# Performance work log

Measured on AMD Instinct MI355X. Metric: run time of the kernel, lower is better.

## Reference

```python
import jax, jax.numpy as jnp
import numpy as np
from jax import lax

DN = ('NCHW', 'OIHW', 'NCHW')

def _conv(x, w, b):
    # Conv2d(k=4, stride=2, padding=1): H -> H/2
    y = lax.conv_general_dilated(x, w, (2, 2), ((1, 1), (1, 1)), dimension_numbers=DN)
    return y + b[None, :, None, None]

def _deconv(x, w, b):
    # ConvTranspose2d(k=4, stride=2, padding=1): H -> 2H.
    # Equivalent dense conv: flip kernel spatially, swap in/out channels,
    # lhs_dilation = stride, padding = k-1-p = 2.
    wf = jnp.flip(w, (2, 3)).transpose(1, 0, 2, 3)  # (out, in, 4, 4)
    y = lax.conv_general_dilated(x, wf, (1, 1), ((2, 2), (2, 2)), lhs_dilation=(2, 2), dimension_numbers=DN)
    return y + b[None, :, None, None]

def setup_inputs() -> dict:
    key = jax.random.key(0)
    ks = jax.random.split(key, 20)
    f = jnp.float32
    s = 0.05  # small init scale for stability
    inp = {
        'x':   jax.random.uniform(ks[0], (64, 3, 224, 224), dtype=f),
        # encoder conv weights (OIHW) + biases
        'ew1': jax.random.normal(ks[1], (32, 3, 4, 4), f) * s,   'eb1': jnp.zeros((32,), f),
        'ew2': jax.random.normal(ks[2], (64, 32, 4, 4), f) * s,  'eb2': jnp.zeros((64,), f),
        'ew3': jax.random.normal(ks[3], (128, 64, 4, 4), f) * s, 'eb3': jnp.zeros((128,), f),
        'ew4': jax.random.normal(ks[4], (64, 128, 4, 4), f) * s, 'eb4': jnp.zeros((64,), f),
        # codebook: uniform(-1/K, 1/K) like torch init, K=4000, D=12544
        'emb': jax.random.uniform(ks[5], (4000, 12544), f, -1.0 / 4000, 1.0 / 4000),
        # decoder conv-transpose weights in torch layout (in, out, kh, kw) + biases
        'dw1': jax.random.normal(ks[6], (64, 128, 4, 4), f) * s, 'db1': jnp.zeros((128,), f),
        'dw2': jax.random.normal(ks[7], (128, 64, 4, 4), f) * s, 'db2': jnp.zeros((64,), f),
        'dw3': jax.random.normal(ks[8], (64, 32, 4, 4), f) * s,  'db3': jnp.zeros((32,), f),
        'dw4': jax.random.normal(ks[9], (32, 3, 4, 4), f) * s,   'db4': jnp.zeros((3,), f),
    }
    return inp

def reference(x, ew1, eb1, ew2, eb2, ew3, eb3, ew4, eb4, emb,
              dw1, db1, dw2, db2, dw3, db3, dw4, db4):
    sg = lax.stop_gradient
    B = x.shape[0]
    # ---- Encoder ----
    h = jax.nn.relu(_conv(x, ew1, eb1))
    h = jax.nn.relu(_conv(h, ew2, eb2))
    h = jax.nn.relu(_conv(h, ew3, eb3))
    h = _conv(h, ew4, eb4)                 # (B, 64, 14, 14)
    z = h.reshape(B, -1)                   # (B, 12544)
    # ---- Vector quantization ----
    # ||z||^2 - 2 z E^T + ||e||^2, argmin over codebook
    dist = (jnp.sum(z * z, axis=1, keepdims=True)
            - 2.0 * (z @ emb.T)
            + jnp.sum(emb * emb, axis=1))  # (B, 4000)
    idx = jnp.argmin(dist, axis=1)         # (B,)
    quantized = emb[idx]                   # (B, 12544) -- direct gather (== onehot @ emb)
    e_latent = jnp.mean((sg(quantized) - z) ** 2)
    q_latent = jnp.mean((quantized - sg(z)) ** 2)
    vq_loss = q_latent + 0.25 * e_latent
    zq = z + sg(quantized - z)             # straight-through
    # ---- Decoder ----
    d = zq.reshape(B, 64, 14, 14)
    d = jax.nn.relu(_deconv(d, dw1, db1))
    d = jax.nn.relu(_deconv(d, dw2, db2))
    d = jax.nn.relu(_deconv(d, dw3, db3))
    x_recon = jax.nn.sigmoid(_deconv(d, dw4, db4))  # (B, 3, 224, 224)
    recon_loss = jnp.mean((x_recon - x) ** 2)
    loss = recon_loss + vq_loss
    return (x_recon, loss, recon_loss, vq_loss)
```

## Files before the change

### kernel.cpp

```cpp
#include <hip/hip_runtime.h>
#include <math.h>

typedef unsigned short u16;
typedef unsigned int u32;
typedef __attribute__((ext_vector_type(8))) short short8;
typedef __attribute__((ext_vector_type(4))) float f32x4;

__device__ __forceinline__ u16 f2bf(float f) {
    u32 u = __float_as_uint(f);
    u = u + 0x7fffu + ((u >> 16) & 1u);
    return (u16)(u >> 16);
}
__device__ __forceinline__ float bf2f(u16 h) { return __uint_as_float(((u32)h) << 16); }

__device__ __forceinline__ f32x4 mfma16(short8 a, short8 b, f32x4 c) {
    return __builtin_amdgcn_mfma_f32_16x16x32_bf16(a, b, c, 0, 0, 0);
}

__device__ __forceinline__ uint4 pack8(float4 a, float4 b) {
    uint4 r;
    r.x = (u32)f2bf(a.x) | ((u32)f2bf(a.y) << 16);
    r.y = (u32)f2bf(a.z) | ((u32)f2bf(a.w) << 16);
    r.z = (u32)f2bf(b.x) | ((u32)f2bf(b.y) << 16);
    r.w = (u32)f2bf(b.z) | ((u32)f2bf(b.w) << 16);
    return r;
}

__global__ __launch_bounds__(256) void prep_conv_w(
    const float* __restrict__ w, u16* __restrict__ o, int CIN, int COUT)
{
    int i = blockIdx.x * 256 + threadIdx.x;
    int tot = CIN * 16 * COUT;
    if (i >= tot) return;
    int j = i & 7; int r = i >> 3;
    int co = r % COUT; int r2 = r / COUT;
    int tap = r2 & 15; int ch = r2 >> 4;
    int ci = ch * 8 + j;
    o[i] = f2bf(w[((size_t)co * CIN + ci) * 16 + tap]);
}
__global__ __launch_bounds__(256) void prep_deconv_w(
    const float* __restrict__ w, u16* __restrict__ o, int CIN, int COUT, int COPAD)
{
    int i = blockIdx.x * 256 + threadIdx.x;
    int tot = CIN * 16 * COPAD;
    if (i >= tot) return;
    int j = i & 7; int r = i >> 3;
    int co = r % COPAD; int r2 = r / COPAD;
    int t16 = r2 & 15; int ch = r2 >> 4;
    int py = t16 >> 3, px = (t16 >> 2) & 1, qq = t16 & 3;
    int ta = qq >> 1, tb = qq & 1;
    int ky = py + 2 * ta, kx = px + 2 * tb;
    int ci = ch * 8 + j;
    o[i] = (co < COUT) ? f2bf(w[(((size_t)ci * COUT + co) * 16) + ky * 4 + kx]) : (u16)0;
}
__global__ __launch_bounds__(256) void prep_conv1_w(
    const float* __restrict__ w, u16* __restrict__ o)
{
    int i = blockIdx.x * 256 + threadIdx.x;
    if (i >= 2048) return;
    int j = i & 7; int kx = j >> 1, cp = j & 1;
    int r = i >> 3;
    int co = r & 31; int r2 = r >> 5;
    int ky = r2 & 3; int h = r2 >> 2;
    int ci = 2 * h + cp;
    o[i] = (ci < 3) ? f2bf(w[((co * 3 + ci) * 16) + ky * 4 + kx]) : (u16)0;
}

template<int CIN, int COUT, int COTILE, int H2, int W2, int NSEG, int MB,
         int MBW, int NWF, int RELU, int STOREZ>
__global__ __launch_bounds__(256) void conv_mfma(
    const u16* __restrict__ in, const u16* __restrict__ wcvt,
    const float* __restrict__ bias, u16* __restrict__ outp,
    float* __restrict__ z32)
{
    constexpr int CHUNKS = CIN / 8, CGI = CIN / 8, CGO = COUT / 8;
    constexpr int HIN = H2 * 2, WIN = W2 * 2, SLOTW = 35;
    constexpr int NF = COTILE / 16, WM = MB / MBW, WN = NF / NWF;
    static_assert(WM * WN == 4, "wave layout");
    constexpr int TBu = MB * 4 * SLOTW, WBu = 16 * COTILE;
    constexpr int EBu = (MB * 16 * COTILE * 2 + 15) / 16;
    constexpr int SM = (TBu + WBu) > EBu ? (TBu + WBu) : EBu;
    __shared__ uint4 smem[SM];
    uint4* T = smem; uint4* wS = smem + TBu;
    u16* E = (u16*)smem;

    const int tid = threadIdx.x, wid = tid >> 6, lane = tid & 63;
    const int q = lane >> 4, lm = lane & 15;
    const int wm = wid / WN, wn = wid % WN;
    const int cobase = blockIdx.y * COTILE;
    const int mbase = blockIdx.x * MB;

    f32x4 acc[MBW][NWF];
    #pragma unroll
    for (int a = 0; a < MBW; ++a)
        #pragma unroll
        for (int b = 0; b < NWF; ++b) {
            acc[a][b][0] = 0.f; acc[a][b][1] = 0.f;
            acc[a][b][2] = 0.f; acc[a][b][3] = 0.f;
        }

    for (int ch = 0; ch < CHUNKS; ++ch) {
        __syncthreads();
        for (int i = tid; i < TBu; i += 256) {
            int mb = i / (4 * SLOTW), r2 = i % (4 * SLOTW);
            int r = r2 / SLOTW, s = r2 % SLOTW;
            int mbg = mbase + mb;
            int n = mbg / (H2 * NSEG), rr = mbg % (H2 * NSEG);
            int oy = rr / NSEG, ox0 = (rr % NSEG) << 4;
            int iy = 2 * oy - 1 + r, ix = 2 * ox0 - 1 + s;
            uint4 v = {0u, 0u, 0u, 0u};
            if ((unsigned)iy < (unsigned)HIN && (unsigned)ix < (unsigned)WIN)
                v = *(const uint4*)(in + (size_t)(((n * CGI + ch) * HIN + iy) * WIN + ix) * 8);
            T[i] = v;
        }
        for (int i = tid; i < WBu; i += 256) {
            int tap = i / COTILE, co = i % COTILE;
            wS[i] = *(const uint4*)(wcvt + (size_t)((ch * 16 + tap) * COUT + cobase + co) * 8);
        }
        __syncthreads();
        #pragma unroll
        for (int ky = 0; ky < 4; ++ky) {
            short8 Af[MBW]; short8 Bf[NWF];
            #pragma unroll
            for (int im = 0; im < MBW; ++im) {
                int mb = wm * MBW + im;
                Af[im] = *(const short8*)(T + (mb * 4 + ky) * SLOTW + 2 * lm + q);
            }
            #pragma unroll
            for (int inf = 0; inf < NWF; ++inf)
                Bf[inf] = *(const short8*)(wS + (ky * 4 + q) * COTILE + wn * NWF * 16 + inf * 16 + lm);
            #pragma unroll
            for (int im = 0; im < MBW; ++im)
                #pragma unroll
                for (int inf = 0; inf < NWF; ++inf)
                    acc[im][inf] = mfma16(Af[im], Bf[inf], acc[im][inf]);
        }
    }
    __syncthreads();
    #pragma unroll
    for (int inf = 0; inf < NWF; ++inf) {
        int col = wn * NWF * 16 + inf * 16 + lm;
        float bv = bias[cobase + col];
        #pragma unroll
        for (int im = 0; im < MBW; ++im) {
            int pixb = (wm * MBW + im) * 16 + q * 4;
            #pragma unroll
            for (int r = 0; r < 4; ++r) {
                float v = acc[im][inf][r] + bv;
                if (RELU) v = fmaxf(v, 0.f);
                E[(pixb + r) * COTILE + col] = f2bf(v);
            }
        }
    }
    __syncthreads();
    for (int i = tid; i < MB * 16 * (COTILE / 8); i += 256) {
        int pix = i / (COTILE / 8), cg = i % (COTILE / 8);
        int mb = pix >> 4, m = pix & 15;
        int mbg = mbase + mb;
        int n = mbg / (H2 * NSEG), rr = mbg % (H2 * NSEG);
        int oy = rr / NSEG, ox0 = (rr % NSEG) << 4;
        int ox = ox0 + m;
        if (ox < W2)
            *(uint4*)(outp + (size_t)(((n * CGO + cobase / 8 + cg) * H2 + oy) * W2 + ox) * 8) =
                *(uint4*)(E + pix * COTILE + cg * 8);
    }
    if (STOREZ) {
        for (int i = tid; i < MB * 16 * COTILE; i += 256) {
            int pix = i / COTILE, co = i % COTILE;
            int mb = pix >> 4, m = pix & 15;
            int mbg = mbase + mb;
            int n = mbg / (H2 * NSEG), rr = mbg % (H2 * NSEG);
            int oy = rr / NSEG, ox0 = (rr % NSEG) << 4;
            int ox = ox0 + m;
            if (ox < W2)
                z32[(size_t)((n * COUT + cobase + co) * H2 + oy) * W2 + ox] =
                    bf2f(E[pix * COTILE + co]);
        }
    }
}

__global__ __launch_bounds__(256) void conv1_mfma(
    const float* __restrict__ x, const u16* __restrict__ w1c,
    const float* __restrict__ bias, u16* __restrict__ outp)
{
    constexpr int MB = 16, MBW = 4, NWF = 2, COTILE = 32, W2 = 112, H2 = 112, NSEG = 7;
    constexpr int TBu = MB * 2 * 64, WBu = 256;
    __shared__ uint4 smem[TBu + WBu];
    uint4* T1 = smem; uint4* w1S = smem + TBu;
    u16* E = (u16*)smem;

    const int tid = threadIdx.x, wid = tid >> 6, lane = tid & 63;
    const int q = lane >> 4, lm = lane & 15;
    const int wm = wid;
    const int mbase = blockIdx.x * MB;

    f32x4 acc[MBW][NWF];
    #pragma unroll
    for (int a = 0; a < MBW; ++a)
        #pragma unroll
        for (int b = 0; b < NWF; ++b) {
            acc[a][b][0] = 0.f; acc[a][b][1] = 0.f;
            acc[a][b][2] = 0.f; acc[a][b][3] = 0.f;
        }

    for (int i = tid; i < TBu; i += 256) {
        int mb = i >> 7; int r = i & 127;
        int h = r >> 6; int r2 = r & 63;
        int ky = r2 >> 4; int m = r2 & 15;
        int mbg = mbase + mb;
        int n = mbg / (H2 * NSEG), rr = mbg % (H2 * NSEG);
        int oy = rr / NSEG, ox0 = (rr % NSEG) << 4;
        int iy = 2 * oy - 1 + ky;
        int ixb = 2 * (ox0 + m) - 1;
        u32 u[4];
        #pragma unroll
        for (int kx = 0; kx < 4; ++kx) {
            float v0 = 0.f, v1 = 0.f;
            int ix = ixb + kx;
            if ((unsigned)iy < 224u && (unsigned)ix < 224u) {
                int ci0 = 2 * h;
                v0 = x[((size_t)(n * 3 + ci0) * 224 + iy) * 224 + ix];
                if (ci0 + 1 < 3) v1 = x[((size_t)(n * 3 + ci0 + 1) * 224 + iy) * 224 + ix];
            }
            u[kx] = (u32)f2bf(v0) | ((u32)f2bf(v1) << 16);
        }
        uint4 vv; vv.x = u[0]; vv.y = u[1]; vv.z = u[2]; vv.w = u[3];
        T1[i] = vv;
    }
    if (tid < 256) {
        w1S[tid] = *(const uint4*)(w1c + (size_t)tid * 8);
    }
    __syncthreads();
    #pragma unroll
    for (int h = 0; h < 2; ++h) {
        short8 Af[MBW]; short8 Bf[NWF];
        #pragma unroll
        for (int im = 0; im < MBW; ++im) {
            int mb = wm * MBW + im;
            Af[im] = *(const short8*)(T1 + (mb * 2 + h) * 64 + lane);
        }
        #pragma unroll
        for (int inf = 0; inf < NWF; ++inf)
            Bf[inf] = *(const short8*)(w1S + (h * 4 + q) * 32 + inf * 16 + lm);
        #pragma unroll
        for (int im = 0; im < MBW; ++im)
            #pragma unroll
            for (int inf = 0; inf < NWF; ++inf)
                acc[im][inf] = mfma16(Af[im], Bf[inf], acc[im][inf]);
    }
    __syncthreads();
    #pragma unroll
    for (int inf = 0; inf < NWF; ++inf) {
        int col = inf * 16 + lm;
        float bv = bias[col];
        #pragma unroll
        for (int im = 0; im < MBW; ++im) {
            int pixb = (wm * MBW + im) * 16 + q * 4;
            #pragma unroll
            for (int r = 0; r < 4; ++r) {
                float v = fmaxf(acc[im][inf][r] + bv, 0.f);
                E[(pixb + r) * COTILE + col] = f2bf(v);
            }
        }
    }
    __syncthreads();
    for (int i = tid; i < MB * 16 * (COTILE / 8); i += 256) {
        int pix = i / (COTILE / 8), cg = i % (COTILE / 8);
        int mb = pix >> 4, m = pix & 15;
        int mbg = mbase + mb;
        int n = mbg / (H2 * NSEG), rr = mbg % (H2 * NSEG);
        int oy = rr / NSEG, ox0 = (rr % NSEG) << 4;
        int ox = ox0 + m;
        *(uint4*)(outp + (size_t)(((n * 4 + cg) * H2 + oy) * W2 + ox) * 8) =
            *(uint4*)(E + pix * COTILE + cg * 8);
    }
}

template<int CIN, int COUT, int COPAD, int COTILE, int Hp, int Wp, int NSEG,
         int MB, int MBW, int NWF, int RELU>
__global__ __launch_bounds__(256) void deconv_mfma(
    const u16* __restrict__ in, const u16* __restrict__ dcvt,
    const float* __restrict__ bias, u16* __restrict__ outp)
{
    constexpr int CHUNKS = CIN / 8, CGI = CIN / 8, CGO = COUT / 8;
    constexpr int SLOTW = 17;
    constexpr int NF = COTILE / 16, WM = MB / MBW, WN = NF / NWF;
    static_assert(WM * WN == 4, "wave layout");
    constexpr int BPP = 64 * Hp * NSEG / MB;
    constexpr int TBu = MB * 2 * SLOTW, WBu = 4 * COTILE;
    constexpr int EBu = (MB * 16 * COTILE * 2 + 15) / 16;
    constexpr int SM = (TBu + WBu) > EBu ? (TBu + WBu) : EBu;
    __shared__ uint4 smem[SM];
    uint4* T = smem; uint4* wS = smem + TBu;
    u16* E = (u16*)smem;

    const int tid = threadIdx.x, wid = tid >> 6, lane = tid & 63;
    const int q = lane >> 4, lm = lane & 15;
    const int wm = wid / WN, wn = wid % WN;
    const int par = blockIdx.x / BPP;
    const int py = par >> 1, px = par & 1;
    const int mbase = (blockIdx.x % BPP) * MB;
    const int cobase = blockIdx.y * COTILE;

    f32x4 acc[MBW][NWF];
    #pragma unroll
    for (int a = 0; a < MBW; ++a)
        #pragma unroll
        for (int b = 0; b < NWF; ++b) {
            acc[a][b][0] = 0.f; acc[a][b][1] = 0.f;
            acc[a][b][2] = 0.f; acc[a][b][3] = 0.f;
        }

    for (int ch = 0; ch < CHUNKS; ++ch) {
        __syncthreads();
        for (int i = tid; i < TBu; i += 256) {
            int mb = i / (2 * SLOTW), r2 = i % (2 * SLOTW);
            int rr_ = r2 / SLOTW, s = r2 % SLOTW;
            int mbg = mbase + mb;
            int n = mbg / (Hp * NSEG), rm = mbg % (Hp * NSEG);
            int oyp = rm / NSEG, u0 = (rm % NSEG) << 4;
            int iy = oyp + (1 - py) - 1 + rr_;
            int ix = u0 + (1 - px) - 1 + s;
            uint4 v = {0u, 0u, 0u, 0u};
            if ((unsigned)iy < (unsigned)Hp && (unsigned)ix < (unsigned)Wp)
                v = *(const uint4*)(in + (size_t)(((n * CGI + ch) * Hp + iy) * Wp + ix) * 8);
            T[i] = v;
        }
        for (int i = tid; i < WBu; i += 256) {
            int qq = i / COTILE, co = i % COTILE;
            wS[i] = *(const uint4*)(dcvt + (size_t)((ch * 16 + par * 4 + qq) * COPAD + cobase + co) * 8);
        }
        __syncthreads();
        {
            short8 Af[MBW]; short8 Bf[NWF];
            #pragma unroll
            for (int im = 0; im < MBW; ++im) {
                int mb = wm * MBW + im;
                Af[im] = *(const short8*)(T + (mb * 2 + (1 - (q >> 1))) * SLOTW + lm + 1 - (q & 1));
            }
            #pragma unroll
            for (int inf = 0; inf < NWF; ++inf)
                Bf[inf] = *(const short8*)(wS + q * COTILE + wn * NWF * 16 + inf * 16 + lm);
            #pragma unroll
            for (int im = 0; im < MBW; ++im)
                #pragma unroll
                for (int inf = 0; inf < NWF; ++inf)
                    acc[im][inf] = mfma16(Af[im], Bf[inf], acc[im][inf]);
        }
    }
    __syncthreads();
    #pragma unroll
    for (int inf = 0; inf < NWF; ++inf) {
        int col = wn * NWF * 16 + inf * 16 + lm;
        float bv = bias[cobase + col];
        #pragma unroll
        for (int im = 0; im < MBW; ++im) {
            int pixb = (wm * MBW + im) * 16 + q * 4;
            #pragma unroll
            for (int r = 0; r < 4; ++r) {
                float v = acc[im][inf][r] + bv;
                if (RELU) v = fmaxf(v, 0.f);
                E[(pixb + r) * COTILE + col] = f2bf(v);
            }
        }
    }
    __syncthreads();
    for (int i = tid; i < MB * 16 * (COTILE / 8); i += 256) {
        int pix = i / (COTILE / 8), cg = i % (COTILE / 8);
        int mb = pix >> 4, m = pix & 15;
        int mbg = mbase + mb;
        int n = mbg / (Hp * NSEG), rm = mbg % (Hp * NSEG);
        int oyp = rm / NSEG, u0 = (rm % NSEG) << 4;
        int u = u0 + m;
        if (u < Wp) {
            int ox = 2 * u + (px ? 0 : 1);
            int oy = 2 * oyp + (py ? 0 : 1);
            *(uint4*)(outp + (size_t)(((n * CGO + cobase / 8 + cg) * (2 * Hp) + oy) * (2 * Wp) + ox) * 8) =
                *(uint4*)(E + pix * COTILE + cg * 8);
        }
    }
}

__global__ __launch_bounds__(256) void deconv4_mfma(
    const u16* __restrict__ in, const u16* __restrict__ dcvt,
    const float* __restrict__ bias, float* __restrict__ outp,
    const float* __restrict__ xref, float* __restrict__ bpart)
{
    constexpr int Hp = 112, Wp = 112, NSEG = 7, MB = 16, MBW = 4;
    constexpr int CGI = 4, CHUNKS = 4, COPAD = 16;
    constexpr int TROW = 3, TCOL = 18;
    constexpr int TBu = MB * TROW * TCOL;
    constexpr int WBu = CHUNKS * 16 * COPAD / 16 * 16;
    __shared__ uint4 smem[TBu + 1024];
    __shared__ float red[4];
    uint4* T = smem; uint4* wS = smem + TBu;

    const int tid = threadIdx.x, wid = tid >> 6, lane = tid & 63;
    const int q = lane >> 4, lm = lane & 15;
    const int wm = wid;
    const int mbase = blockIdx.x * MB;

    f32x4 acc[4][MBW];
    #pragma unroll
    for (int p = 0; p < 4; ++p)
        #pragma unroll
        for (int a = 0; a < MBW; ++a) {
            acc[p][a][0] = 0.f; acc[p][a][1] = 0.f; acc[p][a][2] = 0.f; acc[p][a][3] = 0.f;
        }

    for (int i = tid; i < 1024; i += 256)
        wS[i] = *(const uint4*)(dcvt + (size_t)i * 8);

    for (int ch = 0; ch < CHUNKS; ++ch) {
        __syncthreads();
        for (int i = tid; i < TBu; i += 256) {
            int mb = i / (TROW * TCOL), r2 = i % (TROW * TCOL);
            int r = r2 / TCOL, s = r2 % TCOL;
            int mbg = mbase + mb;
            int n = mbg / (Hp * NSEG), rm = mbg % (Hp * NSEG);
            int oyp = rm / NSEG, u0 = (rm % NSEG) << 4;
            int iy = oyp - 1 + r;
            int ix = u0 - 1 + s;
            uint4 v = {0u, 0u, 0u, 0u};
            if ((unsigned)iy < (unsigned)Hp && (unsigned)ix < (unsigned)Wp)
                v = *(const uint4*)(in + (size_t)(((n * CGI + ch) * Hp + iy) * Wp + ix) * 8);
            T[i] = v;
        }
        __syncthreads();
        #pragma unroll
        for (int par = 0; par < 4; ++par) {
            const int py = par >> 1, px = par & 1;
            short8 Bf = *(const short8*)(wS + (ch * 16 + par * 4 + q) * 16 + lm);
            #pragma unroll
            for (int im = 0; im < MBW; ++im) {
                int mb = wm * MBW + im;
                short8 Af = *(const short8*)(T + (mb * TROW + (2 - py - (q >> 1))) * TCOL
                                             + lm + 2 - px - (q & 1));
                acc[par][im] = mfma16(Af, Bf, acc[par][im]);
            }
        }
    }

    const int co = lm;
    float bv = (co < 3) ? bias[co] : 0.f;
    float lsum = 0.f;
    if (co < 3) {
        #pragma unroll
        for (int im = 0; im < MBW; ++im) {
            int mbg = mbase + wm * MBW + im;
            int n = mbg / (Hp * NSEG), rm = mbg % (Hp * NSEG);
            int oyp = rm / NSEG, u0 = (rm % NSEG) << 4;
            #pragma unroll
            for (int r = 0; r < 4; ++r) {
                int u = u0 + q * 4 + r;
                float v3 = acc[3][im][r] + bv;
                float v2 = acc[2][im][r] + bv;
                float v1 = acc[1][im][r] + bv;
                float v0 = acc[0][im][r] + bv;
                float s3 = 1.f / (1.f + expf(-v3));
                float s2 = 1.f / (1.f + expf(-v2));
                float s1 = 1.f / (1.f + expf(-v1));
                float s0 = 1.f / (1.f + expf(-v0));
                size_t rowA = ((size_t)(n * 3 + co) * 224 + 2 * oyp) * 224 + 2 * u;
                size_t rowB = rowA + 224;
                float2 xa = *(const float2*)(xref + rowA);
                float2 xb = *(const float2*)(xref + rowB);
                *(float2*)(outp + rowA) = make_float2(s3, s2);
                *(float2*)(outp + rowB) = make_float2(s1, s0);
                float d0 = s3 - xa.x, d1 = s2 - xa.y, d2 = s1 - xb.x, d3 = s0 - xb.y;
                lsum += d0 * d0 + d1 * d1 + d2 * d2 + d3 * d3;
            }
        }
    }
    #pragma unroll
    for (int off = 32; off > 0; off >>= 1)
        lsum += __shfl_down(lsum, off, 64);
    if (lane == 0) red[wid] = lsum;
    __syncthreads();
    if (tid == 0)
        bpart[blockIdx.x] = red[0] + red[1] + red[2] + red[3];
}

__global__ __launch_bounds__(256) void vq_gemm(
    const float* __restrict__ z32, const float* __restrict__ emb,
    float* __restrict__ P, float* __restrict__ normp)
{
    __shared__ uint4 As[8 * 64];
    __shared__ uint4 Bs[8 * 256];
    const int tid = threadIdx.x, wid = tid >> 6, lane = tid & 63;
    const int q = lane >> 4, lm = lane & 15;
    const int jt = blockIdx.x, ks = blockIdx.y;
    const int jg = jt * 256 + tid;
    const int jc = jg < 4000 ? jg : 3999;
    const float* brow = emb + (size_t)jc * 12544 + ks * 896;
    const int m = tid & 63, ksub = tid >> 6;
    const float* arow = z32 + (size_t)m * 12544 + ks * 896 + ksub * 16;

    f32x4 acc[4][4];
    #pragma unroll
    for (int a = 0; a < 4; ++a)
        #pragma unroll
        for (int b = 0; b < 4; ++b) {
            acc[a][b][0] = 0.f; acc[a][b][1] = 0.f; acc[a][b][2] = 0.f; acc[a][b][3] = 0.f;
        }
    float nsq = 0.f;

    for (int ch = 0; ch < 14; ++ch) {
        __syncthreads();
        {
            float4 f0 = *(const float4*)(arow + ch * 64);
            float4 f1 = *(const float4*)(arow + ch * 64 + 4);
            float4 f2 = *(const float4*)(arow + ch * 64 + 8);
            float4 f3 = *(const float4*)(arow + ch * 64 + 12);
            As[(ksub * 2 + 0) * 64 + m] = pack8(f0, f1);
            As[(ksub * 2 + 1) * 64 + m] = pack8(f2, f3);
        }
        {
            const float* bp = brow + ch * 64;
            #pragma unroll
            for (int ko = 0; ko < 8; ++ko) {
                float4 fa = *(const float4*)(bp + ko * 8);
                float4 fb = *(const float4*)(bp + ko * 8 + 4);
                nsq += fa.x * fa.x + fa.y * fa.y + fa.z * fa.z + fa.w * fa.w
                     + fb.x * fb.x + fb.y * fb.y + fb.z * fb.z + fb.w * fb.w;
                Bs[ko * 256 + tid] = pack8(fa, fb);
            }
        }
        __syncthreads();
        #pragma unroll
        for (int kk = 0; kk < 2; ++kk) {
            short8 Af[4]; short8 Bf[4];
            #pragma unroll
            for (int mf = 0; mf < 4; ++mf)
                Af[mf] = *(const short8*)(As + (kk * 4 + q) * 64 + mf * 16 + lm);
            #pragma unroll
            for (int nf = 0; nf < 4; ++nf)
                Bf[nf] = *(const short8*)(Bs + (kk * 4 + q) * 256 + wid * 64 + nf * 16 + lm);
            #pragma unroll
            for (int mf = 0; mf < 4; ++mf)
                #pragma unroll
                for (int nf = 0; nf < 4; ++nf)
                    acc[mf][nf] = mfma16(Af[mf], Bf[nf], acc[mf][nf]);
        }
    }
    #pragma unroll
    for (int mf = 0; mf < 4; ++mf)
        #pragma unroll
        for (int nf = 0; nf < 4; ++nf) {
            int j = jt * 256 + wid * 64 + nf * 16 + lm;
            if (j < 4000) {
                #pragma unroll
                for (int r = 0; r < 4; ++r) {
                    int b = mf * 16 + q * 4 + r;
                    P[(size_t)(ks * 64 + b) * 4000 + j] = acc[mf][nf][r];
                }
            }
        }
    if (jg < 4000) normp[ks * 4000 + jg] = nsq;
}

__global__ __launch_bounds__(256) void vq_argmin(
    const float* __restrict__ P, const float* __restrict__ normp,
    int* __restrict__ idxout)
{
    const int b = blockIdx.x;
    const int tid = threadIdx.x;
    float best = 3.4e38f;
    int bidx = 0x7fffffff;
    for (int j = tid; j < 4000; j += 256) {
        float dot = 0.f, nrm = 0.f;
        #pragma unroll
        for (int s = 0; s < 14; ++s) {
            dot += P[(size_t)(s * 64 + b) * 4000 + j];
            nrm += normp[s * 4000 + j];
        }
        float d = nrm - 2.f * dot;
        if (d < best) { best = d; bidx = j; }
    }
    __shared__ float sv[256];
    __shared__ int si[256];
    sv[tid] = best; si[tid] = bidx;
    __syncthreads();
    for (int off = 128; off > 0; off >>= 1) {
        if (tid < off) {
            float v2 = sv[tid + off]; int i2 = si[tid + off];
            if (v2 < sv[tid] || (v2 == sv[tid] && i2 < si[tid])) { sv[tid] = v2; si[tid] = i2; }
        }
        __syncthreads();
    }
    if (tid == 0) idxout[b] = si[0];
}

__global__ __launch_bounds__(256) void vq_gather(
    const float* __restrict__ emb, const float* __restrict__ z32,
    const int* __restrict__ idx, u16* __restrict__ Qb, float* __restrict__ vacc)
{
    const int b = blockIdx.x;
    const int code = idx[b];
    const float* e = emb + (size_t)code * 12544;
    const float* zb = z32 + (size_t)b * 12544;
    float ls = 0.f;
    for (int d = threadIdx.x; d < 12544; d += 256) {
        float ev = e[d];
        int co = d / 196, rem = d % 196;
        int y = rem / 14, xx = rem % 14;
        Qb[((size_t)((b * 8 + (co >> 3)) * 14 + y) * 14 + xx) * 8 + (co & 7)] = f2bf(ev);
        float df = ev - zb[d];
        ls += df * df;
    }
    #pragma unroll
    for (int off = 32; off > 0; off >>= 1)
        ls += __shfl_down(ls, off, 64);
    if ((threadIdx.x & 63) == 0) atomicAdd(vacc, ls);
}

__global__ __launch_bounds__(256) void reduce_final(
    const float* __restrict__ bpart, const float* __restrict__ vacc,
    float* __restrict__ tail)
{
    const int tid = threadIdx.x;
    float s = 0.f;
    for (int i = tid; i < 3136; i += 256) s += bpart[i];
    #pragma unroll
    for (int off = 32; off > 0; off >>= 1)
        s += __shfl_down(s, off, 64);
    __shared__ float red[4];
    if ((tid & 63) == 0) red[tid >> 6] = s;
    __syncthreads();
    if (tid == 0) {
        float rsum = red[0] + red[1] + red[2] + red[3];
        float recon = rsum * (1.f / 9633792.f);
        float vq = 1.25f * vacc[0] * (1.f / 802816.f);
        tail[0] = recon + vq;
        tail[1] = recon;
        tail[2] = vq;
    }
}

extern "C" void kernel_launch(void* const* d_in, const int* in_sizes, int n_in,
                              void* d_out, int out_size, void* d_ws, size_t ws_size,
                              hipStream_t stream)
{
    const float* x   = (const float*)d_in[0];
    const float* ew1 = (const float*)d_in[1];
    const float* eb1 = (const float*)d_in[2];
    const float* ew2 = (const float*)d_in[3];
    const float* eb2 = (const float*)d_in[4];
    const float* ew3 = (const float*)d_in[5];
    const float* eb3 = (const float*)d_in[6];
    const float* ew4 = (const float*)d_in[7];
    const float* eb4 = (const float*)d_in[8];
    const float* emb = (const float*)d_in[9];
    const float* dw1 = (const float*)d_in[10];
    const float* db1 = (const float*)d_in[11];
    const float* dw2 = (const float*)d_in[12];
    const float* db2 = (const float*)d_in[13];
    const float* dw3 = (const float*)d_in[14];
    const float* db3 = (const float*)d_in[15];
    const float* dw4 = (const float*)d_in[16];
    const float* db4 = (const float*)d_in[17];
    float* out = (float*)d_out;

    size_t off = 0;
    char* base = (char*)d_ws;
    auto nxt = [&](size_t bytes) -> char* {
        char* p = base + off;
        off = (off + bytes + 255) & ~(size_t)255;
        return p;
    };
    u16*   A1    = (u16*)nxt(25690112ull * 2);
    u16*   A2    = (u16*)nxt(12845056ull * 2);
    u16*   A3    = (u16*)nxt(6422528ull * 2);
    float* z32   = (float*)nxt(802816ull * 4);
    u16*   Qb    = (u16*)nxt(802816ull * 2);
    float* P     = (float*)nxt(14ull * 64 * 4000 * 4);
    float* normp = (float*)nxt(14ull * 4000 * 4);
    u16*   w1c   = (u16*)nxt(2048ull * 2);
    u16*   wc2   = (u16*)nxt(32768ull * 2);
    u16*   wc3   = (u16*)nxt(131072ull * 2);
    u16*   wc4   = (u16*)nxt(131072ull * 2);
    u16*   wd1   = (u16*)nxt(131072ull * 2);
    u16*   wd2   = (u16*)nxt(131072ull * 2);
    u16*   wd3   = (u16*)nxt(32768ull * 2);
    u16*   wd4   = (u16*)nxt(8192ull * 2);
    float* accp  = (float*)nxt(512);
    int*   idxp  = (int*)nxt(64 * 4);
    float* bpart = (float*)nxt(3136ull * 4);
    u16*   D1 = A3;
    u16*   D2 = A2;
    u16*   D3 = A1;

    hipMemsetAsync(accp, 0, 8, stream);

    prep_conv1_w <<<8,   256, 0, stream>>>(ew1, w1c);
    prep_conv_w  <<<128, 256, 0, stream>>>(ew2, wc2, 32, 64);
    prep_conv_w  <<<512, 256, 0, stream>>>(ew3, wc3, 64, 128);
    prep_conv_w  <<<512, 256, 0, stream>>>(ew4, wc4, 128, 64);
    prep_deconv_w<<<512, 256, 0, stream>>>(dw1, wd1, 64, 128, 128);
    prep_deconv_w<<<512, 256, 0, stream>>>(dw2, wd2, 128, 64, 64);
    prep_deconv_w<<<128, 256, 0, stream>>>(dw3, wd3, 64, 32, 32);
    prep_deconv_w<<<32,  256, 0, stream>>>(dw4, wd4, 32, 3, 16);

    conv1_mfma<<<3136, 256, 0, stream>>>(x, w1c, eb1, A1);
    conv_mfma<32, 64, 64, 56, 56, 4, 16, 8, 2, 1, 0>
        <<<dim3(896, 1), 256, 0, stream>>>(A1, wc2, eb2, A2, nullptr);
    conv_mfma<64, 128, 64, 28, 28, 2, 8, 4, 2, 1, 0>
        <<<dim3(448, 2), 256, 0, stream>>>(A2, wc3, eb3, A3, nullptr);
    conv_mfma<128, 64, 64, 14, 14, 1, 8, 2, 4, 0, 1>
        <<<dim3(112, 1), 256, 0, stream>>>(A3, wc4, eb4, Qb, z32);

    vq_gemm  <<<dim3(16, 14), 256, 0, stream>>>(z32, emb, P, normp);
    vq_argmin<<<64, 256, 0, stream>>>(P, normp, idxp);
    vq_gather<<<64, 256, 0, stream>>>(emb, z32, idxp, Qb, accp);

    deconv_mfma<64, 128, 128, 64, 14, 14, 1, 8, 4, 2, 1>
        <<<dim3(448, 2), 256, 0, stream>>>(Qb, wd1, db1, D1);
    deconv_mfma<128, 64, 64, 64, 28, 28, 2, 16, 8, 2, 1>
        <<<dim3(896, 1), 256, 0, stream>>>(D1, wd2, db2, D2);
    deconv_mfma<64, 32, 32, 32, 56, 56, 4, 16, 8, 1, 1>
        <<<dim3(3584, 1), 256, 0, stream>>>(D2, wd3, db3, D3);
    deconv4_mfma<<<3136, 256, 0, stream>>>(D3, wd4, db4, out, x, bpart);

    reduce_final<<<1, 256, 0, stream>>>(bpart, accp, out + 9633792);
}
```

Baseline: 799.6 us.

## Use direct global-to-LDS loads, fuse prep and VQ kernels, coalesce final store

Replaces register-staged tile and weight loads in the conv and deconv kernels with global_load_lds 16-byte transfers that write straight into shared memory, with zero-filling for out-of-bounds slots. The eight weight-prep kernels are merged into one launch, and argmin is fused with the codebook gather. The last deconv epilogue is staged through LDS so the sigmoid output and the loss read of x use float4 coalesced accesses. Together these aim to cut VGPR traffic, launch overhead and scattered stores. They also depend on the LDS destination layout matching the per-wave lane ordering that global_load_lds uses.

```diff
diff --git a/kernel.cpp b/kernel.cpp
--- a/kernel.cpp
+++ b/kernel.cpp
@@ -26,24 +26,34 @@
     return r;
 }
 
-__global__ __launch_bounds__(256) void prep_conv_w(
-    const float* __restrict__ w, u16* __restrict__ o, int CIN, int COUT)
-{
-    int i = blockIdx.x * 256 + threadIdx.x;
-    int tot = CIN * 16 * COUT;
-    if (i >= tot) return;
+#define GLOAD_LDS16(gsrc, ldst)                                                      \
+    __builtin_amdgcn_global_load_lds(                                                \
+        (__attribute__((address_space(1))) u32*)(gsrc),                              \
+        (__attribute__((address_space(3))) u32*)(ldst), 16, 0, 0)
+
+__device__ __forceinline__ void prep1_item(const float* __restrict__ w,
+                                           u16* __restrict__ o, int i)
+{
+    int j = i & 7; int kx = j >> 1, cp = j & 1;
+    int r = i >> 3;
+    int co = r & 31; int r2 = r >> 5;
+    int ky = r2 & 3; int h = r2 >> 2;
+    int ci = 2 * h + cp;
+    o[i] = (ci < 3) ? f2bf(w[((co * 3 + ci) * 16) + ky * 4 + kx]) : (u16)0;
+}
+__device__ __forceinline__ void prepc_item(const float* __restrict__ w,
+                                           u16* __restrict__ o, int CIN, int COUT, int i)
+{
     int j = i & 7; int r = i >> 3;
     int co = r % COUT; int r2 = r / COUT;
     int tap = r2 & 15; int ch = r2 >> 4;
     int ci = ch * 8 + j;
     o[i] = f2bf(w[((size_t)co * CIN + ci) * 16 + tap]);
 }
-__global__ __launch_bounds__(256) void prep_deconv_w(
-    const float* __restrict__ w, u16* __restrict__ o, int CIN, int COUT, int COPAD)
-{
-    int i = blockIdx.x * 256 + threadIdx.x;
-    int tot = CIN * 16 * COPAD;
-    if (i >= tot) return;
+__device__ __forceinline__ void prepd_item(const float* __restrict__ w,
+                                           u16* __restrict__ o, int CIN, int COUT,
+                                           int COPAD, int i)
+{
     int j = i & 7; int r = i >> 3;
     int co = r % COPAD; int r2 = r / COPAD;
     int t16 = r2 & 15; int ch = r2 >> 4;
@@ -53,17 +63,33 @@
     int ci = ch * 8 + j;
     o[i] = (co < COUT) ? f2bf(w[(((size_t)ci * COUT + co) * 16) + ky * 4 + kx]) : (u16)0;
 }
-__global__ __launch_bounds__(256) void prep_conv1_w(
-    const float* __restrict__ w, u16* __restrict__ o)
+
+__global__ __launch_bounds__(256) void prep_all(
+    const float* __restrict__ ew1, const float* __restrict__ ew2,
+    const float* __restrict__ ew3, const float* __restrict__ ew4,
+    const float* __restrict__ dw1, const float* __restrict__ dw2,
+    const float* __restrict__ dw3, const float* __restrict__ dw4,
+    u16* __restrict__ w1c, u16* __restrict__ wc2,
+    u16* __restrict__ wc3, u16* __restrict__ wc4,
+    u16* __restrict__ wd1, u16* __restrict__ wd2,
+    u16* __restrict__ wd3, u16* __restrict__ wd4)
 {
     int i = blockIdx.x * 256 + threadIdx.x;
-    if (i >= 2048) return;
-    int j = i & 7; int kx = j >> 1, cp = j & 1;
-    int r = i >> 3;
-    int co = r & 31; int r2 = r >> 5;
-    int ky = r2 & 3; int h = r2 >> 2;
-    int ci = 2 * h + cp;
-    o[i] = (ci < 3) ? f2bf(w[((co * 3 + ci) * 16) + ky * 4 + kx]) : (u16)0;
+    if (i < 2048) { prep1_item(ew1, w1c, i); return; }
+    i -= 2048;
+    if (i < 32768)  { prepc_item(ew2, wc2, 32, 64, i); return; }
+    i -= 32768;
+    if (i < 131072) { prepc_item(ew3, wc3, 64, 128, i); return; }
+    i -= 131072;
+    if (i < 131072) { prepc_item(ew4, wc4, 128, 64, i); return; }
+    i -= 131072;
+    if (i < 131072) { prepd_item(dw1, wd1, 64, 128, 128, i); return; }
+    i -= 131072;
+    if (i < 131072) { prepd_item(dw2, wd2, 128, 64, 64, i); return; }
+    i -= 131072;
+    if (i < 32768)  { prepd_item(dw3, wd3, 64, 32, 32, i); return; }
+    i -= 32768;
+    if (i < 8192)   { prepd_item(dw4, wd4, 32, 3, 16, i); return; }
 }
 
 template<int CIN, int COUT, int COTILE, int H2, int W2, int NSEG, int MB,
@@ -101,21 +127,29 @@
 
     for (int ch = 0; ch < CHUNKS; ++ch) {
         __syncthreads();
-        for (int i = tid; i < TBu; i += 256) {
-            int mb = i / (4 * SLOTW), r2 = i % (4 * SLOTW);
-            int r = r2 / SLOTW, s = r2 % SLOTW;
-            int mbg = mbase + mb;
-            int n = mbg / (H2 * NSEG), rr = mbg % (H2 * NSEG);
-            int oy = rr / NSEG, ox0 = (rr % NSEG) << 4;
-            int iy = 2 * oy - 1 + r, ix = 2 * ox0 - 1 + s;
-            uint4 v = {0u, 0u, 0u, 0u};
-            if ((unsigned)iy < (unsigned)HIN && (unsigned)ix < (unsigned)WIN)
-                v = *(const uint4*)(in + (size_t)(((n * CGI + ch) * HIN + iy) * WIN + ix) * 8);
-            T[i] = v;
-        }
-        for (int i = tid; i < WBu; i += 256) {
+        for (int ib = 0; ib < TBu; ib += 256) {
+            int i = ib + tid;
+            uint4* ldst = T + ib + (wid << 6);
+            if (i < TBu) {
+                int mb = i / (4 * SLOTW), r2 = i % (4 * SLOTW);
+                int r = r2 / SLOTW, s = r2 % SLOTW;
+                int mbg = mbase + mb;
+                int n = mbg / (H2 * NSEG), rr = mbg % (H2 * NSEG);
+                int oy = rr / NSEG, ox0 = (rr % NSEG) << 4;
+                int iy = 2 * oy - 1 + r, ix = 2 * ox0 - 1 + s;
+                if ((unsigned)iy < (unsigned)HIN && (unsigned)ix < (unsigned)WIN) {
+                    GLOAD_LDS16(in + (size_t)(((n * CGI + ch) * HIN + iy) * WIN + ix) * 8, ldst);
+                } else {
+                    uint4 zz = {0u, 0u, 0u, 0u};
+                    T[i] = zz;
+                }
+            }
+        }
+        for (int ib = 0; ib < WBu; ib += 256) {
+            int i = ib + tid;
             int tap = i / COTILE, co = i % COTILE;
-            wS[i] = *(const uint4*)(wcvt + (size_t)((ch * 16 + tap) * COUT + cobase + co) * 8);
+            GLOAD_LDS16(wcvt + (size_t)((ch * 16 + tap) * COUT + cobase + co) * 8,
+                        wS + ib + (wid << 6));
         }
         __syncthreads();
         #pragma unroll
@@ -313,22 +347,32 @@
 
     for (int ch = 0; ch < CHUNKS; ++ch) {
         __syncthreads();
-        for (int i = tid; i < TBu; i += 256) {
-            int mb = i / (2 * SLOTW), r2 = i % (2 * SLOTW);
-            int rr_ = r2 / SLOTW, s = r2 % SLOTW;
-            int mbg = mbase + mb;
-            int n = mbg / (Hp * NSEG), rm = mbg % (Hp * NSEG);
-            int oyp = rm / NSEG, u0 = (rm % NSEG) << 4;
-            int iy = oyp + (1 - py) - 1 + rr_;
-            int ix = u0 + (1 - px) - 1 + s;
-            uint4 v = {0u, 0u, 0u, 0u};
-            if ((unsigned)iy < (unsigned)Hp && (unsigned)ix < (unsigned)Wp)
-                v = *(const uint4*)(in + (size_t)(((n * CGI + ch) * Hp + iy) * Wp + ix) * 8);
-            T[i] = v;
-        }
-        for (int i = tid; i < WBu; i += 256) {
-            int qq = i / COTILE, co = i % COTILE;
-            wS[i] = *(const uint4*)(dcvt + (size_t)((ch * 16 + par * 4 + qq) * COPAD + cobase + co) * 8);
+        for (int ib = 0; ib < TBu; ib += 256) {
+            int i = ib + tid;
+            uint4* ldst = T + ib + (wid << 6);
+            if (i < TBu) {
+                int mb = i / (2 * SLOTW), r2 = i % (2 * SLOTW);
+                int rr_ = r2 / SLOTW, s = r2 % SLOTW;
+                int mbg = mbase + mb;
+                int n = mbg / (Hp * NSEG), rm = mbg % (Hp * NSEG);
+                int oyp = rm / NSEG, u0 = (rm % NSEG) << 4;
+                int iy = oyp + (1 - py) - 1 + rr_;
+                int ix = u0 + (1 - px) - 1 + s;
+                if ((unsigned)iy < (unsigned)Hp && (unsigned)ix < (unsigned)Wp) {
+                    GLOAD_LDS16(in + (size_t)(((n * CGI + ch) * Hp + iy) * Wp + ix) * 8, ldst);
+                } else {
+                    uint4 zz = {0u, 0u, 0u, 0u};
+                    T[i] = zz;
+                }
+            }
+        }
+        for (int ib = 0; ib < WBu; ib += 256) {
+            int i = ib + tid;
+            if (i < WBu) {
+                int qq = i / COTILE, co = i % COTILE;
+                GLOAD_LDS16(dcvt + (size_t)((ch * 16 + par * 4 + qq) * COPAD + cobase + co) * 8,
+                            wS + ib + (wid << 6));
+            }
         }
         __syncthreads();
         {
@@ -387,13 +431,13 @@
     const float* __restrict__ xref, float* __restrict__ bpart)
 {
     constexpr int Hp = 112, Wp = 112, NSEG = 7, MB = 16, MBW = 4;
-    constexpr int CGI = 4, CHUNKS = 4, COPAD = 16;
+    constexpr int CGI = 4, CHUNKS = 4;
     constexpr int TROW = 3, TCOL = 18;
     constexpr int TBu = MB * TROW * TCOL;
-    constexpr int WBu = CHUNKS * 16 * COPAD / 16 * 16;
     __shared__ uint4 smem[TBu + 1024];
     __shared__ float red[4];
     uint4* T = smem; uint4* wS = smem + TBu;
+    float* Ef = (float*)smem;
 
     const int tid = threadIdx.x, wid = tid >> 6, lane = tid & 63;
     const int q = lane >> 4, lm = lane & 15;
@@ -408,23 +452,29 @@
             acc[p][a][0] = 0.f; acc[p][a][1] = 0.f; acc[p][a][2] = 0.f; acc[p][a][3] = 0.f;
         }
 
-    for (int i = tid; i < 1024; i += 256)
-        wS[i] = *(const uint4*)(dcvt + (size_t)i * 8);
+    for (int ib = 0; ib < 1024; ib += 256)
+        GLOAD_LDS16(dcvt + (size_t)(ib + tid) * 8, wS + ib + (wid << 6));
 
     for (int ch = 0; ch < CHUNKS; ++ch) {
         __syncthreads();
-        for (int i = tid; i < TBu; i += 256) {
-            int mb = i / (TROW * TCOL), r2 = i % (TROW * TCOL);
-            int r = r2 / TCOL, s = r2 % TCOL;
-            int mbg = mbase + mb;
-            int n = mbg / (Hp * NSEG), rm = mbg % (Hp * NSEG);
-            int oyp = rm / NSEG, u0 = (rm % NSEG) << 4;
-            int iy = oyp - 1 + r;
-            int ix = u0 - 1 + s;
-            uint4 v = {0u, 0u, 0u, 0u};
-            if ((unsigned)iy < (unsigned)Hp && (unsigned)ix < (unsigned)Wp)
-                v = *(const uint4*)(in + (size_t)(((n * CGI + ch) * Hp + iy) * Wp + ix) * 8);
-            T[i] = v;
+        for (int ib = 0; ib < TBu; ib += 256) {
+            int i = ib + tid;
+            uint4* ldst = T + ib + (wid << 6);
+            if (i < TBu) {
+                int mb = i / (TROW * TCOL), r2 = i % (TROW * TCOL);
+                int r = r2 / TCOL, s = r2 % TCOL;
+                int mbg = mbase + mb;
+                int n = mbg / (Hp * NSEG), rm = mbg % (Hp * NSEG);
+                int oyp = rm / NSEG, u0 = (rm % NSEG) << 4;
+                int iy = oyp - 1 + r;
+                int ix = u0 - 1 + s;
+                if ((unsigned)iy < (unsigned)Hp && (unsigned)ix < (unsigned)Wp) {
+                    GLOAD_LDS16(in + (size_t)(((n * CGI + ch) * Hp + iy) * Wp + ix) * 8, ldst);
+                } else {
+                    uint4 zz = {0u, 0u, 0u, 0u};
+                    T[i] = zz;
+                }
+            }
         }
         __syncthreads();
         #pragma unroll
@@ -441,36 +491,45 @@
         }
     }
 
-    const int co = lm;
-    float bv = (co < 3) ? bias[co] : 0.f;
+    __syncthreads();
+    if (lm < 3) {
+        float bv = bias[lm];
+        #pragma unroll
+        for (int par = 0; par < 4; ++par)
+            #pragma unroll
+            for (int im = 0; im < MBW; ++im)
+                #pragma unroll
+                for (int r = 0; r < 4; ++r)
+                    Ef[(((wm * MBW + im) * 16 + q * 4 + r) * 4 + par) * 3 + lm] =
+                        acc[par][im][r] + bv;
+    }
+    __syncthreads();
     float lsum = 0.f;
-    if (co < 3) {
-        #pragma unroll
-        for (int im = 0; im < MBW; ++im) {
-            int mbg = mbase + wm * MBW + im;
-            int n = mbg / (Hp * NSEG), rm = mbg % (Hp * NSEG);
-            int oyp = rm / NSEG, u0 = (rm % NSEG) << 4;
-            #pragma unroll
-            for (int r = 0; r < 4; ++r) {
-                int u = u0 + q * 4 + r;
-                float v3 = acc[3][im][r] + bv;
-                float v2 = acc[2][im][r] + bv;
-                float v1 = acc[1][im][r] + bv;
-                float v0 = acc[0][im][r] + bv;
-                float s3 = 1.f / (1.f + expf(-v3));
-                float s2 = 1.f / (1.f + expf(-v2));
-                float s1 = 1.f / (1.f + expf(-v1));
-                float s0 = 1.f / (1.f + expf(-v0));
-                size_t rowA = ((size_t)(n * 3 + co) * 224 + 2 * oyp) * 224 + 2 * u;
-                size_t rowB = rowA + 224;
-                float2 xa = *(const float2*)(xref + rowA);
-                float2 xb = *(const float2*)(xref + rowB);
-                *(float2*)(outp + rowA) = make_float2(s3, s2);
-                *(float2*)(outp + rowB) = make_float2(s1, s0);
-                float d0 = s3 - xa.x, d1 = s2 - xa.y, d2 = s1 - xb.x, d3 = s0 - xb.y;
-                lsum += d0 * d0 + d1 * d1 + d2 * d2 + d3 * d3;
-            }
-        }
+    #pragma unroll
+    for (int k = 0; k < 3; ++k) {
+        int i = k * 256 + tid;
+        int mb = i / 48, rem = i % 48;
+        int row = rem / 24, rem2 = rem % 24;
+        int co = rem2 / 8, ox4 = rem2 % 8;
+        int mbg = mbase + mb;
+        int n = mbg / (Hp * NSEG), rm = mbg % (Hp * NSEG);
+        int oyp = rm / NSEG, u0 = (rm % NSEG) << 4;
+        int pA = row ? 1 : 3, pB = row ? 0 : 2;
+        int uL = 2 * ox4, uH = uL + 1;
+        float v0 = Ef[((mb * 16 + uL) * 4 + pA) * 3 + co];
+        float v1 = Ef[((mb * 16 + uL) * 4 + pB) * 3 + co];
+        float v2 = Ef[((mb * 16 + uH) * 4 + pA) * 3 + co];
+        float v3 = Ef[((mb * 16 + uH) * 4 + pB) * 3 + co];
+        float4 sv;
+        sv.x = 1.f / (1.f + expf(-v0));
+        sv.y = 1.f / (1.f + expf(-v1));
+        sv.z = 1.f / (1.f + expf(-v2));
+        sv.w = 1.f / (1.f + expf(-v3));
+        size_t ro = ((size_t)(n * 3 + co) * 224 + 2 * oyp + row) * 224 + 2 * u0 + 4 * ox4;
+        float4 x4 = *(const float4*)(xref + ro);
+        *(float4*)(outp + ro) = sv;
+        float d0 = sv.x - x4.x, d1 = sv.y - x4.y, d2 = sv.z - x4.z, d3 = sv.w - x4.w;
+        lsum += d0 * d0 + d1 * d1 + d2 * d2 + d3 * d3;
     }
     #pragma unroll
     for (int off = 32; off > 0; off >>= 1)
@@ -559,9 +618,10 @@
     if (jg < 4000) normp[ks * 4000 + jg] = nsq;
 }
 
-__global__ __launch_bounds__(256) void vq_argmin(
+__global__ __launch_bounds__(256) void vq_argmin_gather(
     const float* __restrict__ P, const float* __restrict__ normp,
-    int* __restrict__ idxout)
+    const float* __restrict__ emb, const float* __restrict__ z32,
+    u16* __restrict__ Qb, float* __restrict__ vacc)
 {
     const int b = blockIdx.x;
     const int tid = threadIdx.x;
@@ -588,19 +648,11 @@
         }
         __syncthreads();
     }
-    if (tid == 0) idxout[b] = si[0];
-}
-
-__global__ __launch_bounds__(256) void vq_gather(
-    const float* __restrict__ emb, const float* __restrict__ z32,
-    const int* __restrict__ idx, u16* __restrict__ Qb, float* __restrict__ vacc)
-{
-    const int b = blockIdx.x;
-    const int code = idx[b];
+    const int code = si[0];
     const float* e = emb + (size_t)code * 12544;
     const float* zb = z32 + (size_t)b * 12544;
     float ls = 0.f;
-    for (int d = threadIdx.x; d < 12544; d += 256) {
+    for (int d = tid; d < 12544; d += 256) {
         float ev = e[d];
         int co = d / 196, rem = d % 196;
         int y = rem / 14, xx = rem % 14;
@@ -611,7 +663,7 @@
     #pragma unroll
     for (int off = 32; off > 0; off >>= 1)
         ls += __shfl_down(ls, off, 64);
-    if ((threadIdx.x & 63) == 0) atomicAdd(vacc, ls);
+    if ((tid & 63) == 0) atomicAdd(vacc, ls);
 }
 
 __global__ __launch_bounds__(256) void reduce_final(
@@ -684,7 +736,6 @@
     u16*   wd3   = (u16*)nxt(32768ull * 2);
     u16*   wd4   = (u16*)nxt(8192ull * 2);
     float* accp  = (float*)nxt(512);
-    int*   idxp  = (int*)nxt(64 * 4);
     float* bpart = (float*)nxt(3136ull * 4);
     u16*   D1 = A3;
     u16*   D2 = A2;
@@ -692,14 +743,8 @@
 
     hipMemsetAsync(accp, 0, 8, stream);
 
-    prep_conv1_w <<<8,   256, 0, stream>>>(ew1, w1c);
-    prep_conv_w  <<<128, 256, 0, stream>>>(ew2, wc2, 32, 64);
-    prep_conv_w  <<<512, 256, 0, stream>>>(ew3, wc3, 64, 128);
-    prep_conv_w  <<<512, 256, 0, stream>>>(ew4, wc4, 128, 64);
-    prep_deconv_w<<<512, 256, 0, stream>>>(dw1, wd1, 64, 128, 128);
-    prep_deconv_w<<<512, 256, 0, stream>>>(dw2, wd2, 128, 64, 64);
-    prep_deconv_w<<<128, 256, 0, stream>>>(dw3, wd3, 64, 32, 32);
-    prep_deconv_w<<<32,  256, 0, stream>>>(dw4, wd4, 32, 3, 16);
+    prep_all<<<2344, 256, 0, stream>>>(ew1, ew2, ew3, ew4, dw1, dw2, dw3, dw4,
+                                       w1c, wc2, wc3, wc4, wd1, wd2, wd3, wd4);
 
     conv1_mfma<<<3136, 256, 0, stream>>>(x, w1c, eb1, A1);
     conv_mfma<32, 64, 64, 56, 56, 4, 16, 8, 2, 1, 0>
@@ -709,9 +754,8 @@
     conv_mfma<128, 64, 64, 14, 14, 1, 8, 2, 4, 0, 1>
         <<<dim3(112, 1), 256, 0, stream>>>(A3, wc4, eb4, Qb, z32);
 
-    vq_gemm  <<<dim3(16, 14), 256, 0, stream>>>(z32, emb, P, normp);
-    vq_argmin<<<64, 256, 0, stream>>>(P, normp, idxp);
-    vq_gather<<<64, 256, 0, stream>>>(emb, z32, idxp, Qb, accp);
+    vq_gemm<<<dim3(16, 14), 256, 0, stream>>>(z32, emb, P, normp);
+    vq_argmin_gather<<<64, 256, 0, stream>>>(P, normp, emb, z32, Qb, accp);
 
     deconv_mfma<64, 128, 128, 64, 14, 14, 1, 8, 4, 2, 1>
         <<<dim3(448, 2), 256, 0, stream>>>(Qb, wd1, db1, D1);
```

Result: faster. 695.5 us (-13.0%).
